# Kernel optimization log

Hardware: AMD Instinct MI355X
Metric: run time of the kernel (lower is better)

## Reference

```python
import jax, jax.numpy as jnp
import numpy as np

B, T, C = 1, 2048, 1024
H = 16
HD = C // H
BLOCK = 2048
NEG = float('-inf')

def setup_inputs() -> dict:
    key = jax.random.key(0)
    ks = jax.random.split(key, 6)
    x = jax.random.normal(ks[0], (B, T, C), dtype=jnp.float32)
    cumulative_scores = jax.random.normal(ks[1], (B, T), dtype=jnp.float32) * 0.1
    padding_mask = jnp.ones((B, T), dtype=jnp.float32)
    token_index = jax.random.randint(ks[2], (B, T), 0, BLOCK).astype(jnp.int64)
    w_attn = jax.random.normal(ks[3], (C, 3 * C), dtype=jnp.float32) * (1.0 / np.sqrt(C))
    b_attn = jnp.zeros((3 * C,), dtype=jnp.float32)
    w_proj = jax.random.normal(ks[4], (C, C), dtype=jnp.float32) * (1.0 / np.sqrt(C))
    b_proj = jnp.zeros((C,), dtype=jnp.float32)
    return dict(x=x, cumulative_scores=cumulative_scores, padding_mask=padding_mask,
                token_index=token_index, w_attn=w_attn, b_attn=b_attn,
                w_proj=w_proj, b_proj=b_proj)

def _rotate_half(z):
    z1, z2 = z[..., : z.shape[-1] // 2], z[..., z.shape[-1] // 2 :]
    return jnp.concatenate((-z2, z1), axis=-1)

def reference(x, cumulative_scores, padding_mask, token_index, w_attn, b_attn, w_proj, b_proj):
    # fused QKV projection
    qkv = x @ w_attn + b_attn                      # (B,T,3C)
    q, k, v = jnp.split(qkv, 3, axis=2)
    q = q.reshape(B, T, H, HD).transpose(0, 2, 1, 3)  # (B,H,T,HD)
    k = k.reshape(B, T, H, HD).transpose(0, 2, 1, 3)
    v = v.reshape(B, T, H, HD).transpose(0, 2, 1, 3)

    # dynamic per-token RoPE positions: global token counts (original scatter
    # broadcasts indices over batch, so counts are global across all batches)
    cnt = jnp.zeros((BLOCK,), jnp.float32).at[token_index.reshape(-1)].add(1.0)
    per_tok = (1.0 / (cnt + 1e-10))[token_index]       # (B,T)
    partial = jnp.cumsum(per_tok, axis=-1)             # (B,T) fractional positions

    inv_freq = 1.0 / (10000.0 ** (jnp.arange(0, HD, 2, dtype=jnp.float32) / HD))
    freqs = partial[..., None] * inv_freq              # (B,T,HD/2)
    emb = jnp.concatenate((freqs, freqs), axis=-1)     # (B,T,HD)
    cos = jnp.cos(emb)[:, None]                        # (B,1,T,HD)
    sin = jnp.sin(emb)[:, None]
    q = q * cos + _rotate_half(q) * sin
    k = k * cos + _rotate_half(k) * sin

    # 'fork' plan: overwrite last channel
    q = q.at[..., -1].set(1.0)
    k = k.at[..., -1].set(jnp.broadcast_to(cumulative_scores[:, None, :], (B, H, T)))

    # additive causal + padding mask (B,T,T)
    causal = jnp.where(jnp.tril(jnp.ones((T, T), jnp.bool_)), 0.0, NEG)
    pm = jnp.take_along_axis(padding_mask, token_index, axis=1)     # (B,T)
    outer = pm[:, :, None] * pm[:, None, :]
    pad_add = jnp.where(outer.astype(jnp.bool_), 0.0, NEG)
    mask = causal[None, :, :] + pad_add                              # (B,T,T)

    # scale v by exp(cumulative_scores)
    v = v * jnp.exp(cumulative_scores)[:, None, :, None]

    scores = jnp.einsum('bhqd,bhkd->bhqk', q, k) / np.sqrt(HD) + mask[:, None]
    probs = jax.nn.softmax(scores, axis=-1)
    y = jnp.einsum('bhqk,bhkd->bhqd', probs, v)        # (B,H,T,HD)
    y = y.transpose(0, 2, 1, 3).reshape(B, T, C)
    return y @ w_proj + b_proj
```

## Files before the change

### kernel.cpp

```cpp
#include <hip/hip_runtime.h>
#include <math.h>

#define T 2048
#define C 1024
#define H 16
#define HD 64
#define N3 (3*C)
#define NBLOCK 2048

typedef __attribute__((ext_vector_type(8))) short bf16x8;
typedef __attribute__((ext_vector_type(4))) float f32x4;

#define MFMA16(a, b, c) __builtin_amdgcn_mfma_f32_16x16x32_bf16((a), (b), (c), 0, 0, 0)

__device__ inline short f2bf(float f) {
    unsigned u; __builtin_memcpy(&u, &f, 4);
    unsigned r = (u + 0x7fffu + ((u >> 16) & 1u)) >> 16;
    return (short)r;
}
__device__ inline float bf2f(short s) {
    unsigned u = ((unsigned)(unsigned short)s) << 16;
    float f; __builtin_memcpy(&f, &u, 4);
    return f;
}

__device__ inline void gload_lds16(const void* g, void* l) {
    __builtin_amdgcn_global_load_lds((const __attribute__((address_space(1))) unsigned int*)g,
                                     (__attribute__((address_space(3))) unsigned int*)l,
                                     16, 0, 0);
}

__global__ __launch_bounds__(256) void pre_kernel(const float* __restrict__ x,
                                                  const float* __restrict__ w_attn,
                                                  const float* __restrict__ w_proj,
                                                  const int* __restrict__ tok,
                                                  const float* __restrict__ padmask,
                                                  short* __restrict__ xb,
                                                  short* __restrict__ wabT,
                                                  short* __restrict__ wpbT,
                                                  float* __restrict__ partial,
                                                  float* __restrict__ pm_tok) {
    int bid = blockIdx.x;
    int tid = threadIdx.x;
    if (bid == 3072) {
        __shared__ float cntS[NBLOCK];
        __shared__ float sums[256];
        #pragma unroll
        for (int j = 0; j < 8; ++j) cntS[tid * 8 + j] = 0.0f;
        __syncthreads();
        int tk[8];
        #pragma unroll
        for (int j = 0; j < 8; ++j) {
            tk[j] = tok[tid * 8 + j];
            atomicAdd(&cntS[tk[j]], 1.0f);
        }
        __syncthreads();
        float vals[8];
        float s = 0.0f;
        #pragma unroll
        for (int j = 0; j < 8; ++j) {
            s += 1.0f / (cntS[tk[j]] + 1e-10f);
            vals[j] = s;
            pm_tok[tid * 8 + j] = padmask[tk[j]];
        }
        sums[tid] = s;
        __syncthreads();
        for (int off = 1; off < 256; off <<= 1) {
            float v = (tid >= off) ? sums[tid - off] : 0.0f;
            __syncthreads();
            sums[tid] += v;
            __syncthreads();
        }
        float offset = (tid > 0) ? sums[tid - 1] : 0.0f;
        #pragma unroll
        for (int j = 0; j < 8; ++j) partial[tid * 8 + j] = offset + vals[j];
        return;
    }
    if (bid < 2048) {
        int i = bid * 1024 + tid * 4;
        float4 v = *(const float4*)(x + i);
        short4 o;
        o.x = f2bf(v.x); o.y = f2bf(v.y); o.z = f2bf(v.z); o.w = f2bf(v.w);
        *(short4*)(xb + i) = o;
        return;
    }
    __shared__ float S[64][65];
    const float* in; short* out; int Kd, Nd, bx, by;
    if (bid < 2816) {
        int b = bid - 2048;
        bx = b % 48; by = b / 48;
        in = w_attn; out = wabT; Kd = C; Nd = N3;
    } else {
        int b = bid - 2816;
        bx = b % 16; by = b / 16;
        in = w_proj; out = wpbT; Kd = C; Nd = C;
    }
    int n0 = bx * 64, k0 = by * 64;
    #pragma unroll
    for (int i = 0; i < 16; ++i) {
        int lin = tid + i * 256;
        int r = lin >> 6, c = lin & 63;
        S[r][c] = in[(size_t)(k0 + r) * Nd + n0 + c];
    }
    __syncthreads();
    #pragma unroll
    for (int i = 0; i < 16; ++i) {
        int lin = tid + i * 256;
        int rn = lin >> 6, ck = lin & 63;
        out[(size_t)(n0 + rn) * Kd + k0 + ck] = f2bf(S[ck][rn]);
    }
}

template <int OUT_BF16, int EPI>
__global__ __launch_bounds__(256) void gemm_bt64(const short* __restrict__ A,
                                                 const short* __restrict__ Bt,
                                                 const float* __restrict__ bias,
                                                 void* __restrict__ Cout,
                                                 int M, int N, int K,
                                                 const float* __restrict__ partial,
                                                 const float* __restrict__ cumsc,
                                                 const float* __restrict__ pm_tok,
                                                 short* __restrict__ vbT) {
    __shared__ alignas(16) short As[2][2][64 * 32];
    __shared__ alignas(16) short Bs[2][2][128 * 32];
    int tid = threadIdx.x;
    int nwg = gridDim.x * gridDim.y;
    int bidl = blockIdx.y * gridDim.x + blockIdx.x;
    int swz = (bidl & 7) * (nwg >> 3) + (bidl >> 3);
    int m0 = (swz / gridDim.x) * 64, n0 = (swz % gridDim.x) * 128;
    int w = tid >> 6, l = tid & 63;
    int wm = (w >> 1) * 32, wn = (w & 1) * 64;
    int lq = l & 15, g = l >> 4;
    int prow = l >> 2, pcol = (l & 3) * 8;
    f32x4 acc[2][4] = {};

    auto stage = [&](int ph, int k0) {
        #pragma unroll
        for (int hf = 0; hf < 2; ++hf) {
            int kk = k0 + hf * 32;
            int rowA = w * 16 + prow;
            gload_lds16(A + (size_t)(m0 + rowA) * K + kk + pcol, As[ph][hf] + w * 512);
            #pragma unroll
            for (int i = 0; i < 2; ++i) {
                int c = w * 2 + i;
                int row = c * 16 + prow;
                gload_lds16(Bt + (size_t)(n0 + row) * K + kk + pcol, Bs[ph][hf] + c * 512);
            }
        }
    };

    int NK = K / 64;
    stage(0, 0);
    __syncthreads();
    for (int t = 0; t < NK; ++t) {
        int ph = t & 1;
        if (t + 1 < NK) stage(ph ^ 1, (t + 1) * 64);
        #pragma unroll
        for (int hf = 0; hf < 2; ++hf) {
            bf16x8 af[2], bfr[4];
            #pragma unroll
            for (int f = 0; f < 2; ++f)
                af[f] = *(const bf16x8*)(As[ph][hf] + (wm + f * 16 + lq) * 32 + g * 8);
            #pragma unroll
            for (int j = 0; j < 4; ++j)
                bfr[j] = *(const bf16x8*)(Bs[ph][hf] + (wn + j * 16 + lq) * 32 + g * 8);
            #pragma unroll
            for (int fi = 0; fi < 2; ++fi)
                #pragma unroll
                for (int fj = 0; fj < 4; ++fj)
                    acc[fi][fj] = MFMA16(af[fi], bfr[fj], acc[fi][fj]);
        }
        __syncthreads();
    }

    if (EPI == 0) {
        #pragma unroll
        for (int fi = 0; fi < 2; ++fi)
            #pragma unroll
            for (int fj = 0; fj < 4; ++fj)
                #pragma unroll
                for (int r = 0; r < 4; ++r) {
                    int m = m0 + wm + fi * 16 + g * 4 + r;
                    int n = n0 + wn + fj * 16 + lq;
                    float v = acc[fi][fj][r] + bias[n];
                    if (OUT_BF16) ((short*)Cout)[(size_t)m * N + n] = f2bf(v);
                    else          ((float*)Cout)[(size_t)m * N + n] = v;
                }
    } else {
        short* Cb = (short*)Cout;
        int cb = n0 + wn;
        int section = cb >> 10;
        float b0 = bias[cb + lq],      b1 = bias[cb + 16 + lq];
        float b2 = bias[cb + 32 + lq], b3 = bias[cb + 48 + lq];
        if (section < 2) {
            bool isQ = (section == 0);
            float inv0 = exp2f(-(float)lq * (13.287712379549449f / 32.0f));
            float inv1 = exp2f(-(float)(lq + 16) * (13.287712379549449f / 32.0f));
            #pragma unroll
            for (int fi = 0; fi < 2; ++fi)
                #pragma unroll
                for (int r = 0; r < 4; ++r) {
                    int trow = m0 + wm + fi * 16 + g * 4 + r;
                    float pt = partial[trow];
                    float sn0, cs0, sn1, cs1;
                    __sincosf(pt * inv0, &sn0, &cs0);
                    __sincosf(pt * inv1, &sn1, &cs1);
                    float a0 = acc[fi][0][r] + b0;
                    float a1 = acc[fi][1][r] + b1;
                    float a2 = acc[fi][2][r] + b2;
                    float a3 = acc[fi][3][r] + b3;
                    float lo0 = a0 * cs0 - a2 * sn0;
                    float hi0 = a2 * cs0 + a0 * sn0;
                    float lo1 = a1 * cs1 - a3 * sn1;
                    float hi1 = a3 * cs1 + a1 * sn1;
                    if (lq == 15) {
                        float pm = pm_tok[trow];
                        hi1 = isQ ? ((pm != 0.0f) ? 1.0f : 0.0f)
                                  : ((pm != 0.0f) ? cumsc[trow] : -1e20f);
                    }
                    size_t base = (size_t)trow * N3 + cb;
                    Cb[base + lq]      = f2bf(lo0);
                    Cb[base + 16 + lq] = f2bf(lo1);
                    Cb[base + 32 + lq] = f2bf(hi0);
                    Cb[base + 48 + lq] = f2bf(hi1);
                }
        } else {
            int h = (cb - 2 * C) >> 6;
            #pragma unroll
            for (int fi = 0; fi < 2; ++fi) {
                int tb = m0 + wm + fi * 16 + g * 4;
                float ef[4];
                #pragma unroll
                for (int r = 0; r < 4; ++r) ef[r] = __expf(cumsc[tb + r]);
                #pragma unroll
                for (int fj = 0; fj < 4; ++fj) {
                    int d = fj * 16 + lq;
                    float bv = (fj == 0) ? b0 : (fj == 1) ? b1 : (fj == 2) ? b2 : b3;
                    short4 o;
                    o.x = f2bf((acc[fi][fj][0] + bv) * ef[0]);
                    o.y = f2bf((acc[fi][fj][1] + bv) * ef[1]);
                    o.z = f2bf((acc[fi][fj][2] + bv) * ef[2]);
                    o.w = f2bf((acc[fi][fj][3] + bv) * ef[3]);
                    *(short4*)(vbT + (size_t)(h * 64 + d) * T + tb) = o;
                }
            }
        }
    }
}

__global__ __launch_bounds__(256) void attn_flash(const short* __restrict__ qkvb,
                                                  const short* __restrict__ vbT,
                                                  short* __restrict__ yb,
                                                  short* __restrict__ Opart,
                                                  float* __restrict__ Lpart) {
    __shared__ alignas(16) short Kt[2][64 * 64];
    __shared__ alignas(16) short Vt[2][64 * 64];
    __shared__ alignas(16) short Ps[4][16][72];

    int b = blockIdx.x;
    int h, qt, t0, t1, mode;
    if (b < 256)      { h = b & 15; qt = 16 + (b >> 4); t0 = 0;  t1 = 16; mode = 1; }
    else if (b < 512) { int c = b - 256; h = c & 15; qt = 31 - (c >> 4); t0 = 17; t1 = qt; mode = 2; }
    else              { int c = b - 512; h = c & 15; qt = c >> 4; t0 = 0; t1 = qt; mode = 0; }
    int nt = t1 - t0 + 1;

    int tid = threadIdx.x;
    int w = tid >> 6, l = tid & 63;
    int lq = l & 15, g = l >> 4;
    int qrl = w * 16 + lq;
    int qrow = qt * 64 + qrl;

    const short* qbase = qkvb + (size_t)qrow * N3 + h * 64;
    bf16x8 qf0 = *(const bf16x8*)(qbase + g * 8);
    bf16x8 qf1 = *(const bf16x8*)(qbase + 32 + g * 8);

    f32x4 accO[4] = {};
    float lsum = 0.0f;

    int srow = tid >> 3, scol = (tid & 7) * 8;
    const short* kgb = qkvb + C + h * 64 + scol;
    const short* vgb = vbT + (size_t)(h * 64) * T + scol;
    int wb0 = srow * 128 + ((scol * 2) ^ ((srow & 7) << 4));
    int wb1 = (srow + 32) * 128 + ((scol * 2) ^ ((srow & 7) << 4));

    uint4 kr0, kr1, vr0, vr1;
    auto stageRegs = [&](int tile) {
        int kb = tile * 64;
        kr0 = *(const uint4*)(kgb + (size_t)(kb + srow) * N3);
        kr1 = *(const uint4*)(kgb + (size_t)(kb + srow + 32) * N3);
        vr0 = *(const uint4*)(vgb + (size_t)srow * T + kb);
        vr1 = *(const uint4*)(vgb + (size_t)(srow + 32) * T + kb);
    };
    auto writeLds = [&](int buf) {
        *(uint4*)((char*)Kt[buf] + wb0) = kr0;
        *(uint4*)((char*)Kt[buf] + wb1) = kr1;
        *(uint4*)((char*)Vt[buf] + wb0) = vr0;
        *(uint4*)((char*)Vt[buf] + wb1) = vr1;
    };

    auto do_tile = [&](int buf, bool masked) {
        const char* Kc = (const char*)Kt[buf];
        const char* Vc = (const char*)Vt[buf];
        f32x4 s[4] = {};
        __builtin_amdgcn_s_setprio(1);
        #pragma unroll
        for (int f = 0; f < 4; ++f) {
            int row = f * 16 + lq;
            const char* kr_ = Kc + row * 128;
            int sw = (row & 7) << 4;
            bf16x8 a0 = *(const bf16x8*)(kr_ + ((g * 16) ^ sw));
            bf16x8 a1 = *(const bf16x8*)(kr_ + ((64 + g * 16) ^ sw));
            s[f] = MFMA16(a0, qf0, s[f]);
            s[f] = MFMA16(a1, qf1, s[f]);
        }
        __builtin_amdgcn_s_setprio(0);
        float p[16];
        #pragma unroll
        for (int f = 0; f < 4; ++f)
            #pragma unroll
            for (int r = 0; r < 4; ++r) {
                float sv = s[f][r] * 0.125f;
                if (masked) {
                    int kl = f * 16 + g * 4 + r;
                    sv = (kl > qrl) ? -INFINITY : sv;
                }
                float pv = __expf(sv);
                p[f * 4 + r] = pv;
                lsum += pv;
            }
        #pragma unroll
        for (int f = 0; f < 4; ++f) {
            unsigned u0, u1;
            asm("v_cvt_pk_bf16_f32 %0, %1, %2" : "=v"(u0) : "v"(p[f * 4 + 0]), "v"(p[f * 4 + 1]));
            asm("v_cvt_pk_bf16_f32 %0, %1, %2" : "=v"(u1) : "v"(p[f * 4 + 2]), "v"(p[f * 4 + 3]));
            uint2 uu; uu.x = u0; uu.y = u1;
            *(uint2*)&Ps[w][lq][f * 16 + g * 4] = uu;
        }
        __builtin_amdgcn_s_setprio(1);
        #pragma unroll
        for (int kh = 0; kh < 2; ++kh) {
            bf16x8 pa = *(const bf16x8*)&Ps[w][lq][kh * 32 + g * 8];
            #pragma unroll
            for (int f = 0; f < 4; ++f) {
                int vrow = f * 16 + lq;
                const char* vr_ = Vc + vrow * 128;
                bf16x8 vb = *(const bf16x8*)(vr_ + (((kh * 32 + g * 8) * 2) ^ ((vrow & 7) << 4)));
                accO[f] = MFMA16(pa, vb, accO[f]);
            }
        }
        __builtin_amdgcn_s_setprio(0);
    };

    if (nt > 0) { stageRegs(t0); writeLds(0); }
    __syncthreads();

    for (int j = 0; j < nt; ++j) {
        int t = t0 + j;
        bool pf = (j + 1 < nt);
        if (pf) stageRegs(t + 1);
        do_tile(j & 1, t == qt);
        if (pf) writeLds((j & 1) ^ 1);
        __syncthreads();
    }

    lsum += __shfl_xor(lsum, 16);
    lsum += __shfl_xor(lsum, 32);

    if (mode == 0) {
        float linv_own = 1.0f / lsum;
        float li[4];
        #pragma unroll
        for (int r = 0; r < 4; ++r) li[r] = __shfl(linv_own, g * 4 + r);
        #pragma unroll
        for (int f = 0; f < 4; ++f)
            #pragma unroll
            for (int r = 0; r < 4; ++r) {
                int trow = qt * 64 + w * 16 + g * 4 + r;
                yb[(size_t)trow * C + h * 64 + f * 16 + lq] = f2bf(accO[f][r] * li[r]);
            }
    } else {
        int kh = mode - 1;
        int slab = h * 16 + (qt - 16);
        short* Ob = Opart + ((size_t)kh * 256 + slab) * 4096;
        #pragma unroll
        for (int f = 0; f < 4; ++f)
            #pragma unroll
            for (int r = 0; r < 4; ++r)
                Ob[(w * 16 + g * 4 + r) * 64 + f * 16 + lq] = f2bf(accO[f][r]);
        if (g == 0) Lpart[((size_t)kh * 256 + slab) * 64 + w * 16 + lq] = lsum;
    }
}

__global__ __launch_bounds__(256) void attn_combine(const short* __restrict__ Opart,
                                                    const float* __restrict__ Lpart,
                                                    short* __restrict__ yb) {
    __shared__ float linvS[64];
    int s = blockIdx.x;
    int h = s >> 4, qt = 16 + (s & 15);
    int tid = threadIdx.x;
    if (tid < 64)
        linvS[tid] = 1.0f / (Lpart[(size_t)s * 64 + tid] + Lpart[(size_t)(256 + s) * 64 + tid]);
    __syncthreads();
    const short* O0 = Opart + (size_t)s * 4096;
    const short* O1 = Opart + (size_t)(256 + s) * 4096;
    #pragma unroll
    for (int e = 0; e < 2; ++e) {
        int base = tid * 8 + e * 2048;
        bf16x8 a = *(const bf16x8*)(O0 + base);
        bf16x8 c = *(const bf16x8*)(O1 + base);
        int q = base >> 6, d = base & 63;
        float li = linvS[q];
        bf16x8 o;
        #pragma unroll
        for (int i = 0; i < 8; ++i) o[i] = f2bf((bf2f(a[i]) + bf2f(c[i])) * li);
        *(bf16x8*)(yb + (size_t)(qt * 64 + q) * C + h * 64 + d) = o;
    }
}

extern "C" void kernel_launch(void* const* d_in, const int* in_sizes, int n_in,
                              void* d_out, int out_size, void* d_ws, size_t ws_size,
                              hipStream_t stream) {
    const float* x       = (const float*)d_in[0];
    const float* cumsc   = (const float*)d_in[1];
    const float* padmask = (const float*)d_in[2];
    const int*   tok     = (const int*)d_in[3];
    const float* w_attn  = (const float*)d_in[4];
    const float* b_attn  = (const float*)d_in[5];
    const float* w_proj  = (const float*)d_in[6];
    const float* b_proj  = (const float*)d_in[7];
    float* out = (float*)d_out;

    float* part   = (float*)d_ws;
    float* pm_tok = part + 2048;
    float* Lpart  = pm_tok + 2048;
    short* Opart  = (short*)(Lpart + 2 * 256 * 64);
    short* xb     = Opart + (size_t)2 * 256 * 4096;
    short* wabT   = xb + (size_t)T * C;
    short* wpbT   = wabT + (size_t)N3 * C;
    short* qkvb   = wpbT + (size_t)C * C;
    short* vbT    = qkvb + (size_t)T * N3;
    short* yb     = vbT + (size_t)C * T;

    pre_kernel<<<3073, 256, 0, stream>>>(x, w_attn, w_proj, tok, padmask,
                                         xb, wabT, wpbT, part, pm_tok);
    gemm_bt64<1, 1><<<dim3(N3 / 128, T / 64), 256, 0, stream>>>(
        xb, wabT, b_attn, qkvb, T, N3, C, part, cumsc, pm_tok, vbT);
    attn_flash<<<768, 256, 0, stream>>>(qkvb, vbT, yb, Opart, Lpart);
    attn_combine<<<256, 256, 0, stream>>>(Opart, Lpart, yb);
    gemm_bt64<0, 0><<<dim3(C / 128, T / 64), 256, 0, stream>>>(
        yb, wpbT, b_proj, out, T, C, C, nullptr, nullptr, nullptr, nullptr);
}
```

Before: 78.58 us.

## Fuse split-K attention combine into output projection GEMM A-tile loads

Removes the separate attn_combine kernel. The output projection GEMM now builds its A tiles for the second half of query rows directly from the two partial attention outputs and their normalizers, computing the normalized sum in registers before writing it to LDS. The prescan block is also moved to block 0 of the pre-kernel so it is scheduled first. This saves one launch and one round trip of yb through global memory. In exchange those GEMM blocks use synchronous loads plus conversion work instead of asynchronous global-to-LDS loads, which may weaken load/compute overlap in their main loop.

```diff
diff --git a/kernel.cpp b/kernel.cpp
--- a/kernel.cpp
+++ b/kernel.cpp
@@ -42,7 +42,7 @@
                                                   float* __restrict__ pm_tok) {
     int bid = blockIdx.x;
     int tid = threadIdx.x;
-    if (bid == 3072) {
+    if (bid == 0) {
         __shared__ float cntS[NBLOCK];
         __shared__ float sums[256];
         #pragma unroll
@@ -76,8 +76,8 @@
         for (int j = 0; j < 8; ++j) partial[tid * 8 + j] = offset + vals[j];
         return;
     }
-    if (bid < 2048) {
-        int i = bid * 1024 + tid * 4;
+    if (bid < 2049) {
+        int i = (bid - 1) * 1024 + tid * 4;
         float4 v = *(const float4*)(x + i);
         short4 o;
         o.x = f2bf(v.x); o.y = f2bf(v.y); o.z = f2bf(v.z); o.w = f2bf(v.w);
@@ -86,12 +86,12 @@
     }
     __shared__ float S[64][65];
     const float* in; short* out; int Kd, Nd, bx, by;
-    if (bid < 2816) {
-        int b = bid - 2048;
+    if (bid < 2817) {
+        int b = bid - 2049;
         bx = b % 48; by = b / 48;
         in = w_attn; out = wabT; Kd = C; Nd = N3;
     } else {
-        int b = bid - 2816;
+        int b = bid - 2817;
         bx = b % 16; by = b / 16;
         in = w_proj; out = wpbT; Kd = C; Nd = C;
     }
@@ -123,6 +123,7 @@
                                                  short* __restrict__ vbT) {
     __shared__ alignas(16) short As[2][2][64 * 32];
     __shared__ alignas(16) short Bs[2][2][128 * 32];
+    __shared__ float linvS[EPI == 2 ? 16 : 1][64];
     int tid = threadIdx.x;
     int nwg = gridDim.x * gridDim.y;
     int bidl = blockIdx.y * gridDim.x + blockIdx.x;
@@ -134,12 +135,39 @@
     int prow = l >> 2, pcol = (l & 3) * 8;
     f32x4 acc[2][4] = {};
 
+    bool fuseA = (EPI == 2) && (m0 >= 1024);
+    if (fuseA) {
+        int qt16 = (m0 >> 6) - 16;
+        #pragma unroll
+        for (int e = 0; e < 4; ++e) {
+            int idx = tid * 4 + e;
+            int hh = idx >> 6, q = idx & 63;
+            int s = hh * 16 + qt16;
+            linvS[hh][q] = 1.0f / (partial[s * 64 + q] + partial[(256 + s) * 64 + q]);
+        }
+    }
+    if (EPI == 2) __syncthreads();
+
     auto stage = [&](int ph, int k0) {
         #pragma unroll
         for (int hf = 0; hf < 2; ++hf) {
             int kk = k0 + hf * 32;
             int rowA = w * 16 + prow;
-            gload_lds16(A + (size_t)(m0 + rowA) * K + kk + pcol, As[ph][hf] + w * 512);
+            if (fuseA) {
+                int hh = k0 >> 6;
+                int s = hh * 16 + ((m0 >> 6) - 16);
+                int dcol = hf * 32 + pcol;
+                size_t off = (size_t)s * 4096 + rowA * 64 + dcol;
+                bf16x8 a = *(const bf16x8*)(vbT + off);
+                bf16x8 b2 = *(const bf16x8*)(vbT + (size_t)256 * 4096 + off);
+                float li = linvS[hh][rowA];
+                bf16x8 o;
+                #pragma unroll
+                for (int i = 0; i < 8; ++i) o[i] = f2bf((bf2f(a[i]) + bf2f(b2[i])) * li);
+                *(bf16x8*)(As[ph][hf] + rowA * 32 + pcol) = o;
+            } else {
+                gload_lds16(A + (size_t)(m0 + rowA) * K + kk + pcol, As[ph][hf] + w * 512);
+            }
             #pragma unroll
             for (int i = 0; i < 2; ++i) {
                 int c = w * 2 + i;
@@ -173,7 +201,7 @@
         __syncthreads();
     }
 
-    if (EPI == 0) {
+    if (EPI != 1) {
         #pragma unroll
         for (int fi = 0; fi < 2; ++fi)
             #pragma unroll
@@ -391,32 +419,6 @@
     }
 }
 
-__global__ __launch_bounds__(256) void attn_combine(const short* __restrict__ Opart,
-                                                    const float* __restrict__ Lpart,
-                                                    short* __restrict__ yb) {
-    __shared__ float linvS[64];
-    int s = blockIdx.x;
-    int h = s >> 4, qt = 16 + (s & 15);
-    int tid = threadIdx.x;
-    if (tid < 64)
-        linvS[tid] = 1.0f / (Lpart[(size_t)s * 64 + tid] + Lpart[(size_t)(256 + s) * 64 + tid]);
-    __syncthreads();
-    const short* O0 = Opart + (size_t)s * 4096;
-    const short* O1 = Opart + (size_t)(256 + s) * 4096;
-    #pragma unroll
-    for (int e = 0; e < 2; ++e) {
-        int base = tid * 8 + e * 2048;
-        bf16x8 a = *(const bf16x8*)(O0 + base);
-        bf16x8 c = *(const bf16x8*)(O1 + base);
-        int q = base >> 6, d = base & 63;
-        float li = linvS[q];
-        bf16x8 o;
-        #pragma unroll
-        for (int i = 0; i < 8; ++i) o[i] = f2bf((bf2f(a[i]) + bf2f(c[i])) * li);
-        *(bf16x8*)(yb + (size_t)(qt * 64 + q) * C + h * 64 + d) = o;
-    }
-}
-
 extern "C" void kernel_launch(void* const* d_in, const int* in_sizes, int n_in,
                               void* d_out, int out_size, void* d_ws, size_t ws_size,
                               hipStream_t stream) {
@@ -446,7 +448,6 @@
     gemm_bt64<1, 1><<<dim3(N3 / 128, T / 64), 256, 0, stream>>>(
         xb, wabT, b_attn, qkvb, T, N3, C, part, cumsc, pm_tok, vbT);
     attn_flash<<<768, 256, 0, stream>>>(qkvb, vbT, yb, Opart, Lpart);
-    attn_combine<<<256, 256, 0, stream>>>(Opart, Lpart, yb);
-    gemm_bt64<0, 0><<<dim3(C / 128, T / 64), 256, 0, stream>>>(
-        yb, wpbT, b_proj, out, T, C, C, nullptr, nullptr, nullptr, nullptr);
-}
+    gemm_bt64<0, 2><<<dim3(C / 128, T / 64), 256, 0, stream>>>(
+        yb, wpbT, b_proj, out, T, C, C, Lpart, nullptr, nullptr, Opart);
+}
```

Result: slower. 83.63 us (+6.4%).
